# Kernel tuning notes

Hardware: AMD Instinct MI355X
Metric: run time of the kernel (lower is better)

Reference implementation:

```python
import jax, jax.numpy as jnp
import numpy as np

N_HEAD = 16
HEAD_DIM = 64
D_MODEL = N_HEAD * HEAD_DIM  # 1024
B, L = 2, 2048

def setup_inputs() -> dict:
    key = jax.random.key(0)
    k1, k2, k3, k4, k5 = jax.random.split(key, 5)
    s = 0.02
    return {
        "hidden_states": jax.random.normal(k1, (B, L, D_MODEL), dtype=jnp.float32),
        "W_qkv": jax.random.normal(k2, (D_MODEL, 3 * D_MODEL), dtype=jnp.float32) * s,
        "b_qkv": jax.random.normal(k3, (3 * D_MODEL,), dtype=jnp.float32) * s,
        "W_proj": jax.random.normal(k4, (D_MODEL, D_MODEL), dtype=jnp.float32) * s,
        "b_proj": jax.random.normal(k5, (D_MODEL,), dtype=jnp.float32) * s,
        "window_size": 128,
    }

def reference(hidden_states, W_qkv, b_qkv, W_proj, b_proj, window_size):
    Bb, Ll, Dd = hidden_states.shape
    # GPT-2 Conv1D: x @ W + b
    qkv = hidden_states @ W_qkv + b_qkv  # [B, L, 3D]
    q, k, v = jnp.split(qkv, 3, axis=2)
    def to_heads(t):
        return t.reshape(Bb, Ll, N_HEAD, HEAD_DIM).transpose(0, 2, 1, 3)  # [B,H,L,d]
    q, k, v = to_heads(q), to_heads(k), to_heads(v)
    scale = jnp.sqrt(jnp.asarray(HEAD_DIM, dtype=q.dtype))
    scores = jnp.einsum('bhqd,bhkd->bhqk', q, k) / scale  # [B,H,L,L]
    pos = jnp.arange(Ll)
    dist = pos[:, None] - pos[None, :]  # query - key
    sw_mask = (dist < 0) | (dist >= window_size)  # True = masked out
    scores = jnp.where(sw_mask[None, None, :, :], jnp.asarray(-jnp.inf, scores.dtype), scores)
    attn_weights = jax.nn.softmax(scores, axis=-1)  # dropout is identity (eval)
    out = jnp.einsum('bhqk,bhkd->bhqd', attn_weights, v)  # [B,H,L,d]
    out = out.transpose(0, 2, 1, 3).reshape(Bb, Ll, Dd)
    out = out @ W_proj + b_proj
    return (out, attn_weights)
```

## Files before the change

### kernel.cpp

```cpp
#include <hip/hip_runtime.h>
#include <stdint.h>

#define NH 16
#define HD 64
#define DM 1024
#define BB 2
#define LL 2048

typedef __bf16 bf16x8 __attribute__((ext_vector_type(8)));
typedef float f32x4 __attribute__((ext_vector_type(4)));

__device__ __forceinline__ uint16_t f2bf(float f) {
  union { float f; uint32_t u; } x{f};
  uint32_t r = (x.u + 0x7fff + ((x.u >> 16) & 1)) >> 16;
  return (uint16_t)r;
}

__device__ __forceinline__ void gload_lds16(const void* g, void* l) {
  __builtin_amdgcn_global_load_lds(
      (const __attribute__((address_space(1))) unsigned int*)g,
      (__attribute__((address_space(3))) unsigned int*)l, 16, 0, 0);
}

__global__ __launch_bounds__(256) void cvt_bf16(
    const float* __restrict__ x, uint16_t* __restrict__ y, int n4) {
  int i = blockIdx.x * 256 + threadIdx.x;
  if (i >= n4) return;
  float4 v = ((const float4*)x)[i];
  ushort4 o;
  o.x = f2bf(v.x); o.y = f2bf(v.y); o.z = f2bf(v.z); o.w = f2bf(v.w);
  ((ushort4*)y)[i] = o;
}

__global__ __launch_bounds__(256) void transpose_cvt(
    const float* __restrict__ W, uint16_t* __restrict__ WT, int K, int N) {
  __shared__ float t[32][33];
  int bk = blockIdx.y * 32, bn = blockIdx.x * 32;
  int c = threadIdx.x & 31, r0 = threadIdx.x >> 5;
#pragma unroll
  for (int p = 0; p < 4; ++p) {
    int r = r0 + p * 8;
    t[r][c] = W[(size_t)(bk + r) * N + bn + c];
  }
  __syncthreads();
#pragma unroll
  for (int p = 0; p < 4; ++p) {
    int r = r0 + p * 8;
    WT[(size_t)(bn + r) * K + bk + c] = f2bf(t[c][r]);
  }
}

__global__ __launch_bounds__(256) void gemm_bt_bf16(
    const uint16_t* __restrict__ A, const uint16_t* __restrict__ BT,
    const float* __restrict__ bias, float* __restrict__ C,
    int M, int N, int K) {
  __shared__ uint16_t As[128 * 32];
  __shared__ uint16_t Bs[128 * 32];
  const int tid = threadIdx.x;
  const int bm = blockIdx.y * 128, bn = blockIdx.x * 128;
  const int lane = tid & 63, wave = tid >> 6;
  const int wr = wave >> 1, wc = wave & 1;
  f32x4 acc[4][4] = {};

  for (int k0 = 0; k0 < K; k0 += 32) {
#pragma unroll
    for (int c = 0; c < 2; ++c) {
      int e = c * 2048 + tid * 8;
      int r = e >> 5, col = e & 31;
      gload_lds16(A + (size_t)(bm + r) * K + k0 + col, (char*)As + (size_t)e * 2);
      gload_lds16(BT + (size_t)(bn + r) * K + k0 + col, (char*)Bs + (size_t)e * 2);
    }
    __syncthreads();

    const int kseg = (lane >> 4) * 8;
    bf16x8 af[4], bfr[4];
#pragma unroll
    for (int i = 0; i < 4; ++i)
      af[i] = *(const bf16x8*)&As[(wr * 64 + i * 16 + (lane & 15)) * 32 + kseg];
#pragma unroll
    for (int j = 0; j < 4; ++j)
      bfr[j] = *(const bf16x8*)&Bs[(wc * 64 + j * 16 + (lane & 15)) * 32 + kseg];
#pragma unroll
    for (int i = 0; i < 4; ++i)
#pragma unroll
      for (int j = 0; j < 4; ++j)
        acc[i][j] = __builtin_amdgcn_mfma_f32_16x16x32_bf16(af[i], bfr[j], acc[i][j], 0, 0, 0);
    __syncthreads();
  }

#pragma unroll
  for (int i = 0; i < 4; ++i) {
#pragma unroll
    for (int j = 0; j < 4; ++j) {
      int col = bn + wc * 64 + j * 16 + (lane & 15);
      float bv = bias[col];
#pragma unroll
      for (int r = 0; r < 4; ++r) {
        int row = bm + wr * 64 + i * 16 + (lane >> 4) * 4 + r;
        C[(size_t)row * N + col] = acc[i][j][r] + bv;
      }
    }
  }
}

#define QT 32
#define KT 160
#define KPAD 68
#define PPAD 168

__global__ __launch_bounds__(256) void attn_sw(
    const float* __restrict__ qkv,
    float* __restrict__ attnw,
    uint16_t* __restrict__ ctxb,
    const int* __restrict__ wsz_p) {
  __shared__ float Ks[KT][KPAD];
  __shared__ float Ps[QT][PPAD];
  const int wsz = *wsz_p;
  const int tid = threadIdx.x;
  const int ntile = LL / QT;
  const int qt = blockIdx.x % ntile;
  const int h = (blockIdx.x / ntile) % NH;
  const int b = blockIdx.x / (ntile * NH);
  const int q0 = qt * QT;
  const int kmin = max(0, q0 - (wsz - 1));
  const int kbase = kmin & ~31;
  const int nk = q0 + QT - kbase;

  {
    const int c4 = (tid & 15) * 4;
    const int r0 = tid >> 4;
#pragma unroll
    for (int p = 0; p < KT / 16; ++p) {
      int r = r0 + p * 16;
      float4 kv = {0.f, 0.f, 0.f, 0.f};
      if (r < nk)
        kv = *(const float4*)&qkv[(size_t)(b * LL + kbase + r) * (3 * DM) + DM + h * HD + c4];
      *(float4*)&Ks[r][c4] = kv;
    }
  }
  __syncthreads();

  {
    const int qi = tid >> 3;
    const int kg = tid & 7;
    const int q = q0 + qi;
    const float4* qrow4 = (const float4*)(qkv + (size_t)(b * LL + q) * (3 * DM) + h * HD);
    float s[20] = {};
#pragma unroll 4
    for (int d4 = 0; d4 < 16; ++d4) {
      float4 qv = qrow4[d4];
#pragma unroll
      for (int j = 0; j < 20; ++j) {
        float4 kv = *(const float4*)&Ks[kg + 8 * j][d4 * 4];
        s[j] = fmaf(qv.x, kv.x, fmaf(qv.y, kv.y, fmaf(qv.z, kv.z, fmaf(qv.w, kv.w, s[j]))));
      }
    }
    float m = -1e30f;
#pragma unroll
    for (int j = 0; j < 20; ++j) {
      int gk = kbase + kg + 8 * j;
      bool valid = (gk <= q) && (gk > q - wsz);
      s[j] = valid ? s[j] * 0.125f : -1e30f;
      m = fmaxf(m, s[j]);
    }
#pragma unroll
    for (int off = 1; off < 8; off <<= 1)
      m = fmaxf(m, __shfl_xor(m, off, 64));
    float l = 0.f;
#pragma unroll
    for (int j = 0; j < 20; ++j) {
      float e = (s[j] > -1e29f) ? __expf(s[j] - m) : 0.f;
      s[j] = e;
      l += e;
    }
#pragma unroll
    for (int off = 1; off < 8; off <<= 1)
      l += __shfl_xor(l, off, 64);
    float inv = 1.f / l;
#pragma unroll
    for (int j = 0; j < 20; ++j)
      Ps[qi][kg + 8 * j] = s[j] * inv;
  }
  __syncthreads();

  {
#pragma unroll
    for (int it = 0; it < 16; ++it) {
      int r = it * 2 + (tid >> 7);
      size_t rowoff = ((size_t)((b * NH + h) * LL + q0 + r)) * LL;
      int cb = (tid & 127) * 4;
#pragma unroll
      for (int jj = 0; jj < 4; ++jj) {
        int c4 = cb + jj * 512;
        f32x4 v = {0.f, 0.f, 0.f, 0.f};
        int pc = c4 - kbase;
        if (pc >= 0 && pc < KT)
          v = *(const f32x4*)&Ps[r][pc];
        __builtin_nontemporal_store(v, (f32x4*)&attnw[rowoff + c4]);
      }
    }
  }

  {
    const int d = tid & 63;
    const int qb = tid >> 6;
    float acc[8] = {};
    const float* vbase = qkv + (size_t)(b * LL + kbase) * (3 * DM) + 2 * DM + h * HD + d;
#pragma unroll 2
    for (int kk4 = 0; kk4 < KT / 4; ++kk4) {
      float v0 = vbase[(size_t)(4 * kk4 + 0) * (3 * DM)];
      float v1 = vbase[(size_t)(4 * kk4 + 1) * (3 * DM)];
      float v2 = vbase[(size_t)(4 * kk4 + 2) * (3 * DM)];
      float v3 = vbase[(size_t)(4 * kk4 + 3) * (3 * DM)];
#pragma unroll
      for (int i = 0; i < 8; ++i) {
        float4 p = *(const float4*)&Ps[qb + 4 * i][kk4 * 4];
        acc[i] = fmaf(p.x, v0, fmaf(p.y, v1, fmaf(p.z, v2, fmaf(p.w, v3, acc[i]))));
      }
    }
#pragma unroll
    for (int i = 0; i < 8; ++i) {
      int qi = qb + 4 * i;
      ctxb[(size_t)(b * LL + q0 + qi) * DM + h * HD + d] = f2bf(acc[i]);
    }
  }
}

extern "C" void kernel_launch(void* const* d_in, const int* in_sizes, int n_in,
                              void* d_out, int out_size, void* d_ws, size_t ws_size,
                              hipStream_t stream) {
  const float* hs    = (const float*)d_in[0];
  const float* Wqkv  = (const float*)d_in[1];
  const float* bqkv  = (const float*)d_in[2];
  const float* Wproj = (const float*)d_in[3];
  const float* bproj = (const float*)d_in[4];
  const int*   wszp  = (const int*)d_in[5];

  float* out   = (float*)d_out;
  float* attnw = (float*)d_out + (size_t)BB * LL * DM;

  char* wsb = (char*)d_ws;
  float*    qkv    = (float*)wsb;
  uint16_t* hsctxb = (uint16_t*)(wsb + 50331648);
  uint16_t* WqkvT  = (uint16_t*)(wsb + 50331648 + 8388608);
  uint16_t* WprojT = (uint16_t*)(wsb + 50331648 + 8388608 + 6291456);

  dim3 blk(256);

  cvt_bf16<<<dim3((BB * LL * DM / 4 + 255) / 256), blk, 0, stream>>>(hs, hsctxb, BB * LL * DM / 4);
  transpose_cvt<<<dim3(3 * DM / 32, DM / 32), blk, 0, stream>>>(Wqkv, WqkvT, DM, 3 * DM);
  transpose_cvt<<<dim3(DM / 32, DM / 32), blk, 0, stream>>>(Wproj, WprojT, DM, DM);

  gemm_bt_bf16<<<dim3(3 * DM / 128, BB * LL / 128), blk, 0, stream>>>(
      hsctxb, WqkvT, bqkv, qkv, BB * LL, 3 * DM, DM);

  attn_sw<<<dim3(BB * NH * (LL / QT)), blk, 0, stream>>>(qkv, attnw, hsctxb, wszp);

  gemm_bt_bf16<<<dim3(DM / 128, BB * LL / 128), blk, 0, stream>>>(
      hsctxb, WprojT, bproj, out, BB * LL, DM, DM);
}
```

Measured before the change: 695.5 us.

## Use bf16 MFMA for QK^T and PV in sliding-window attention kernel

Replaces the scalar fp32 FMA loops for the score computation and the probability-times-V product with bf16 MFMA 16x16x32 instructions, staging Q and K as bf16 in shared memory. Scores are written to a float buffer that aliases the K staging area, and a bf16 copy of the probabilities is kept for the PV MFMA. V is loaded and converted to bf16 per lane directly from global memory. A launch-bounds occupancy hint is added. This trades fp32 precision in QK and PV for matrix-core throughput. The attention-weights output is still fp32 but computed from bf16 scores.

```diff
diff --git a/kernel.cpp b/kernel.cpp
--- a/kernel.cpp
+++ b/kernel.cpp
@@ -105,18 +105,23 @@
 
 #define QT 32
 #define KT 160
-#define KPAD 68
-#define PPAD 168
-
-__global__ __launch_bounds__(256) void attn_sw(
+#define KS 72
+#define PS 168
+
+__global__ __launch_bounds__(256, 4) void attn_sw(
     const float* __restrict__ qkv,
     float* __restrict__ attnw,
     uint16_t* __restrict__ ctxb,
     const int* __restrict__ wsz_p) {
-  __shared__ float Ks[KT][KPAD];
-  __shared__ float Ps[QT][PPAD];
+  __shared__ __align__(16) char smemU[KT * KS * 2];
+  __shared__ __align__(16) uint16_t Qs[QT * KS];
+  __shared__ __align__(16) uint16_t Psb[QT * PS];
+  uint16_t* Ksb = (uint16_t*)smemU;
+  float* Sf = (float*)smemU;
+
   const int wsz = *wsz_p;
   const int tid = threadIdx.x;
+  const int lane = tid & 63, wave = tid >> 6;
   const int ntile = LL / QT;
   const int qt = blockIdx.x % ntile;
   const int h = (blockIdx.x / ntile) % NH;
@@ -124,19 +129,57 @@
   const int q0 = qt * QT;
   const int kmin = max(0, q0 - (wsz - 1));
   const int kbase = kmin & ~31;
-  const int nk = q0 + QT - kbase;
-
-  {
-    const int c4 = (tid & 15) * 4;
-    const int r0 = tid >> 4;
-#pragma unroll
-    for (int p = 0; p < KT / 16; ++p) {
-      int r = r0 + p * 16;
-      float4 kv = {0.f, 0.f, 0.f, 0.f};
-      if (r < nk)
-        kv = *(const float4*)&qkv[(size_t)(b * LL + kbase + r) * (3 * DM) + DM + h * HD + c4];
-      *(float4*)&Ks[r][c4] = kv;
-    }
+
+  {
+    int r = tid >> 3, c = (tid & 7) * 8;
+    const float* src = qkv + (size_t)(b * LL + q0 + r) * (3 * DM) + h * HD + c;
+    float4 a = *(const float4*)src, b4 = *(const float4*)(src + 4);
+    uint16_t* dst = &Qs[r * KS + c];
+    dst[0] = f2bf(a.x); dst[1] = f2bf(a.y); dst[2] = f2bf(a.z); dst[3] = f2bf(a.w);
+    dst[4] = f2bf(b4.x); dst[5] = f2bf(b4.y); dst[6] = f2bf(b4.z); dst[7] = f2bf(b4.w);
+  }
+#pragma unroll
+  for (int p = 0; p < 3; ++p) {
+    int u = tid + p * 256;
+    int r = u >> 2, c = (u & 3) * 16;
+    if (r < KT) {
+      const float* src = qkv + (size_t)(b * LL + kbase + r) * (3 * DM) + DM + h * HD + c;
+      float4 a = *(const float4*)src, b4 = *(const float4*)(src + 4);
+      float4 e = *(const float4*)(src + 8), f = *(const float4*)(src + 12);
+      uint16_t* dst = &Ksb[r * KS + c];
+      dst[0] = f2bf(a.x); dst[1] = f2bf(a.y); dst[2] = f2bf(a.z); dst[3] = f2bf(a.w);
+      dst[4] = f2bf(b4.x); dst[5] = f2bf(b4.y); dst[6] = f2bf(b4.z); dst[7] = f2bf(b4.w);
+      dst[8] = f2bf(e.x); dst[9] = f2bf(e.y); dst[10] = f2bf(e.z); dst[11] = f2bf(e.w);
+      dst[12] = f2bf(f.x); dst[13] = f2bf(f.y); dst[14] = f2bf(f.z); dst[15] = f2bf(f.w);
+    }
+  }
+  __syncthreads();
+
+  const int mt = wave & 1, ntb = (wave >> 1) * 5;
+  f32x4 sfrag[5];
+  {
+    const int kseg = (lane >> 4) * 8;
+    bf16x8 aq0 = *(const bf16x8*)&Qs[(mt * 16 + (lane & 15)) * KS + kseg];
+    bf16x8 aq1 = *(const bf16x8*)&Qs[(mt * 16 + (lane & 15)) * KS + 32 + kseg];
+#pragma unroll
+    for (int t = 0; t < 5; ++t) {
+      int nt = ntb + t;
+      bf16x8 bk0 = *(const bf16x8*)&Ksb[(nt * 16 + (lane & 15)) * KS + kseg];
+      bf16x8 bk1 = *(const bf16x8*)&Ksb[(nt * 16 + (lane & 15)) * KS + 32 + kseg];
+      f32x4 c = {0.f, 0.f, 0.f, 0.f};
+      c = __builtin_amdgcn_mfma_f32_16x16x32_bf16(aq0, bk0, c, 0, 0, 0);
+      c = __builtin_amdgcn_mfma_f32_16x16x32_bf16(aq1, bk1, c, 0, 0, 0);
+      sfrag[t] = c;
+    }
+  }
+  __syncthreads();
+
+#pragma unroll
+  for (int t = 0; t < 5; ++t) {
+    int nt = ntb + t;
+#pragma unroll
+    for (int r = 0; r < 4; ++r)
+      Sf[(mt * 16 + (lane >> 4) * 4 + r) * PS + nt * 16 + (lane & 15)] = sfrag[t][r];
   }
   __syncthreads();
 
@@ -144,17 +187,9 @@
     const int qi = tid >> 3;
     const int kg = tid & 7;
     const int q = q0 + qi;
-    const float4* qrow4 = (const float4*)(qkv + (size_t)(b * LL + q) * (3 * DM) + h * HD);
-    float s[20] = {};
-#pragma unroll 4
-    for (int d4 = 0; d4 < 16; ++d4) {
-      float4 qv = qrow4[d4];
-#pragma unroll
-      for (int j = 0; j < 20; ++j) {
-        float4 kv = *(const float4*)&Ks[kg + 8 * j][d4 * 4];
-        s[j] = fmaf(qv.x, kv.x, fmaf(qv.y, kv.y, fmaf(qv.z, kv.z, fmaf(qv.w, kv.w, s[j]))));
-      }
-    }
+    float s[20];
+#pragma unroll
+    for (int j = 0; j < 20; ++j) s[j] = Sf[qi * PS + kg + 8 * j];
     float m = -1e30f;
 #pragma unroll
     for (int j = 0; j < 20; ++j) {
@@ -178,8 +213,11 @@
       l += __shfl_xor(l, off, 64);
     float inv = 1.f / l;
 #pragma unroll
-    for (int j = 0; j < 20; ++j)
-      Ps[qi][kg + 8 * j] = s[j] * inv;
+    for (int j = 0; j < 20; ++j) {
+      float p = s[j] * inv;
+      Sf[qi * PS + kg + 8 * j] = p;
+      Psb[qi * PS + kg + 8 * j] = f2bf(p);
+    }
   }
   __syncthreads();
 
@@ -195,34 +233,37 @@
         f32x4 v = {0.f, 0.f, 0.f, 0.f};
         int pc = c4 - kbase;
         if (pc >= 0 && pc < KT)
-          v = *(const f32x4*)&Ps[r][pc];
+          v = *(const f32x4*)&Sf[r * PS + pc];
         __builtin_nontemporal_store(v, (f32x4*)&attnw[rowoff + c4]);
       }
     }
   }
 
   {
-    const int d = tid & 63;
-    const int qb = tid >> 6;
-    float acc[8] = {};
-    const float* vbase = qkv + (size_t)(b * LL + kbase) * (3 * DM) + 2 * DM + h * HD + d;
-#pragma unroll 2
-    for (int kk4 = 0; kk4 < KT / 4; ++kk4) {
-      float v0 = vbase[(size_t)(4 * kk4 + 0) * (3 * DM)];
-      float v1 = vbase[(size_t)(4 * kk4 + 1) * (3 * DM)];
-      float v2 = vbase[(size_t)(4 * kk4 + 2) * (3 * DM)];
-      float v3 = vbase[(size_t)(4 * kk4 + 3) * (3 * DM)];
-#pragma unroll
-      for (int i = 0; i < 8; ++i) {
-        float4 p = *(const float4*)&Ps[qb + 4 * i][kk4 * 4];
-        acc[i] = fmaf(p.x, v0, fmaf(p.y, v1, fmaf(p.z, v2, fmaf(p.w, v3, acc[i]))));
+    const int nt = wave;
+    const int kseg = (lane >> 4) * 8;
+    f32x4 ofrag[2] = {};
+#pragma unroll
+    for (int ks = 0; ks < 5; ++ks) {
+      const float* vs = qkv + (size_t)(b * LL + kbase + ks * 32 + kseg) * (3 * DM) +
+                        2 * DM + h * HD + nt * 16 + (lane & 15);
+      uint16_t vb[8];
+#pragma unroll
+      for (int j = 0; j < 8; ++j) vb[j] = f2bf(vs[(size_t)j * (3 * DM)]);
+      bf16x8 bv = *(const bf16x8*)vb;
+#pragma unroll
+      for (int m = 0; m < 2; ++m) {
+        bf16x8 ap = *(const bf16x8*)&Psb[(m * 16 + (lane & 15)) * PS + ks * 32 + kseg];
+        ofrag[m] = __builtin_amdgcn_mfma_f32_16x16x32_bf16(ap, bv, ofrag[m], 0, 0, 0);
       }
     }
 #pragma unroll
-    for (int i = 0; i < 8; ++i) {
-      int qi = qb + 4 * i;
-      ctxb[(size_t)(b * LL + q0 + qi) * DM + h * HD + d] = f2bf(acc[i]);
-    }
+    for (int m = 0; m < 2; ++m)
+#pragma unroll
+      for (int r = 0; r < 4; ++r) {
+        int q = q0 + m * 16 + (lane >> 4) * 4 + r;
+        ctxb[(size_t)(b * LL + q) * DM + h * HD + nt * 16 + (lane & 15)] = f2bf(ofrag[m][r]);
+      }
   }
 }
 
```

Measured after the change: 638.2 us. 8.2% less time.
